# Optimization experiments

Hardware: AMD Instinct MI355X
Metric: run time of the kernel (lower is better)

Reference implementation:

```python
import math
import jax, jax.numpy as jnp
import numpy as np

B, N, M, C, H = 64, 64, 64, 512, 8
HD = C // H
FREQ = 256  # frequency_embedding_size
MAX_PERIOD = 10000.0


def setup_inputs() -> dict:
    key = jax.random.key(0)
    ks = jax.random.split(key, 10)
    s = 1.0 / math.sqrt(C)
    sf = 1.0 / math.sqrt(FREQ)
    return {
        "query": jax.random.normal(ks[0], (B, N, C), jnp.float32),
        "query_pos": jax.random.uniform(ks[1], (1, N, M), jnp.float32),
        # projection weights stored as [in, out]
        "Wq": jax.random.normal(ks[2], (C, C), jnp.float32) * s,
        "bq": jnp.zeros((C,), jnp.float32),
        "Wk": jax.random.normal(ks[3], (C, C), jnp.float32) * s,  # no bias
        "Wv": jax.random.normal(ks[4], (C, C), jnp.float32) * s,
        "bv": jnp.zeros((C,), jnp.float32),
        "Wo": jax.random.normal(ks[5], (C, C), jnp.float32) * s,
        "bo": jnp.zeros((C,), jnp.float32),
        # ScalarEmbedder MLP: Linear(FREQ->C), SiLU, Linear(C->C)
        "W1": jax.random.normal(ks[6], (FREQ, C), jnp.float32) * sf,
        "b1": jnp.zeros((C,), jnp.float32),
        "W2": jax.random.normal(ks[7], (C, C), jnp.float32) * s,
        "b2": jnp.zeros((C,), jnp.float32),
    }


def _freqs():
    half = FREQ // 2
    return jnp.exp(-math.log(MAX_PERIOD) * jnp.arange(half, dtype=jnp.float32) / half)


def reference(query, query_pos, Wq, bq, Wk, Wv, bv, Wo, bo, W1, b1, W2, b2):
    Bq, Nq, Cq = query.shape
    Mk = query_pos.shape[-1]
    # --- ScalarEmbedder on flattened pairwise positions: [N*M] -> [N*M, C]
    t = query_pos.reshape(-1)                       # [Bp*N*M], Bp = 1
    tf = t[:, None] * _freqs()[None, :]             # [N*M, FREQ/2]
    emb = jnp.concatenate([jnp.cos(tf), jnp.sin(tf)], axis=-1)  # [N*M, FREQ]
    pe = jax.nn.silu(emb @ W1 + b1) @ W2 + b2        # [N*M, C]
    pe = pe.reshape(Nq, Mk, H, HD).transpose(2, 0, 1, 3)  # [H, N, M, hd] (tiled over B via broadcast)

    q = (query @ Wq + bq).reshape(Bq, Nq, H, HD)     # bnhd
    k = (query @ Wk).reshape(Bq, Mk, H, HD)          # bmhd (key = query)
    v = (query @ Wv + bv).reshape(Bq, Mk, H, HD)

    scale = HD ** -0.5
    # attn[b,h,n,m] = sum_d q[b,n,h,d] * pe[h,n,m,d] * k[b,m,h,d]
    scores = jnp.einsum("bnhd,hnmd,bmhd->bhnm", q, pe, k) * scale
    attn = jax.nn.softmax(scores, axis=-1)
    x = jnp.einsum("bhnm,bmhd->bnhd", attn, v).reshape(Bq, Nq, Cq)
    return x @ Wo + bo + query  # identity = query
```

## Files before the change

### kernel.cpp

```cpp
#include <hip/hip_runtime.h>
#include <hip/hip_bf16.h>
#include <math.h>

typedef short short8 __attribute__((ext_vector_type(8)));
typedef float floatx4 __attribute__((ext_vector_type(4)));

__device__ __forceinline__ ushort f2bf(float f) {
    __hip_bfloat16 h = __float2bfloat16(f);
    return *reinterpret_cast<ushort*>(&h);
}
__device__ __forceinline__ void bf8_to_f32(uint4 u, float* f) {
    f[0] = __uint_as_float(u.x << 16); f[1] = __uint_as_float(u.x & 0xffff0000u);
    f[2] = __uint_as_float(u.y << 16); f[3] = __uint_as_float(u.y & 0xffff0000u);
    f[4] = __uint_as_float(u.z << 16); f[5] = __uint_as_float(u.z & 0xffff0000u);
    f[6] = __uint_as_float(u.w << 16); f[7] = __uint_as_float(u.w & 0xffff0000u);
}

#define GLDS16(g, l) __builtin_amdgcn_global_load_lds( \
    (const __attribute__((address_space(1))) void*)(g), \
    (__attribute__((address_space(3))) void*)(l), 16, 0, 0)

__global__ __launch_bounds__(256) void prep_kernel(
        const float* __restrict__ W1, const float* __restrict__ W2,
        const float* __restrict__ Wq, const float* __restrict__ Wk,
        const float* __restrict__ Wv, const float* __restrict__ Wo,
        const float* __restrict__ bq, const float* __restrict__ bv,
        const float* __restrict__ query, const float* __restrict__ qpos,
        ushort* __restrict__ W1t, ushort* __restrict__ W2t,
        ushort* __restrict__ Wqkvt, ushort* __restrict__ Wot,
        ushort* __restrict__ queryB, ushort* __restrict__ embB,
        float* __restrict__ biasC) {
    const int z = blockIdx.z;
    const int tx = threadIdx.x, ty = threadIdx.y;
    const int tid = ty * 32 + tx;
    if (z < 6) {
        const float* src; ushort* dst; int R;
        switch (z) {
            case 0:  src = W1; dst = W1t;              R = 256; break;
            case 1:  src = W2; dst = W2t;              R = 512; break;
            case 2:  src = Wq; dst = Wqkvt;            R = 512; break;
            case 3:  src = Wk; dst = Wqkvt + 512*512;  R = 512; break;
            case 4:  src = Wv; dst = Wqkvt + 1024*512; R = 512; break;
            default: src = Wo; dst = Wot;              R = 512; break;
        }
        const int r0 = blockIdx.y * 32, c0 = blockIdx.x * 32;
        if (r0 >= R) return;
        __shared__ float t[32][33];
        for (int i = ty; i < 32; i += 8) t[i][tx] = src[(size_t)(r0 + i) * 512 + c0 + tx];
        __syncthreads();
        for (int i = ty; i < 32; i += 8) dst[(size_t)(c0 + i) * R + r0 + tx] = f2bf(t[tx][i]);
    } else if (z == 6) {
        const int bid = blockIdx.y * 16 + blockIdx.x;
#pragma unroll
        for (int i = 0; i < 8; ++i) {
            size_t idx4 = (size_t)bid * 2048 + i * 256 + tid;
            float4 v = *(const float4*)(query + idx4 * 4);
            ushort4 o; o.x = f2bf(v.x); o.y = f2bf(v.y); o.z = f2bf(v.z); o.w = f2bf(v.w);
            *(ushort4*)(queryB + idx4 * 4) = o;
        }
        if (bid == 0) {
            for (int i = tid; i < 1536; i += 256)
                biasC[i] = (i < 512) ? bq[i] : ((i < 1024) ? 0.0f : bv[i - 1024]);
        }
    } else {
        const int bid = blockIdx.y * 16 + blockIdx.x;
        const int gt = bid * 256 + tid;
        const int e0 = gt * 16;
        const int r = e0 >> 8, j0 = e0 & 255;
        const float t = qpos[r];
        ushort o[16];
#pragma unroll
        for (int u = 0; u < 16; ++u) {
            int j = j0 + u, i = j & 127;
            float freq = __expf(-9.210340371976184f * (float)i * (1.0f / 128.0f));
            float a = t * freq;
            o[u] = f2bf((j < 128) ? __cosf(a) : __sinf(a));
        }
        *(uint4*)(embB + e0)     = *(uint4*)&o[0];
        *(uint4*)(embB + e0 + 8) = *(uint4*)&o[8];
    }
}

__global__ __launch_bounds__(256) void gemm_bf16(
        const ushort* __restrict__ A, const ushort* __restrict__ Bt,
        const float* __restrict__ bias, const float* __restrict__ resid,
        void* __restrict__ Cout, int M, int N, int K, int act, int out_fp32) {
    __shared__ ushort As[64 * 32];
    __shared__ ushort Bs[64 * 32];
    const int tid = threadIdx.x;
    const int l = tid & 63, w = tid >> 6;
    const int wr = w >> 1, wc = w & 1;
    const int row0 = blockIdx.x * 64, col0 = blockIdx.y * 64;
    const int l15 = l & 15, quad = l >> 4;
    const int arow = w * 16 + (l >> 2), koff = (l & 3) * 8;

    const ushort* gA = A  + (size_t)(row0 + arow) * K + koff;
    const ushort* gB = Bt + (size_t)(col0 + arow) * K + koff;
    ushort* lA = &As[w * 512 + l * 8];
    ushort* lB = &Bs[w * 512 + l * 8];

    floatx4 acc[2][2] = {};

    for (int k0 = 0; k0 < K; k0 += 32) {
        __syncthreads();
        GLDS16(gA + k0, lA);
        GLDS16(gB + k0, lB);
        __syncthreads();
        short8 a0 = *(const short8*)&As[(wr * 32 + l15) * 32 + quad * 8];
        short8 a1 = *(const short8*)&As[(wr * 32 + 16 + l15) * 32 + quad * 8];
        short8 b0 = *(const short8*)&Bs[(wc * 32 + l15) * 32 + quad * 8];
        short8 b1 = *(const short8*)&Bs[(wc * 32 + 16 + l15) * 32 + quad * 8];
        acc[0][0] = __builtin_amdgcn_mfma_f32_16x16x32_bf16(a0, b0, acc[0][0], 0, 0, 0);
        acc[0][1] = __builtin_amdgcn_mfma_f32_16x16x32_bf16(a0, b1, acc[0][1], 0, 0, 0);
        acc[1][0] = __builtin_amdgcn_mfma_f32_16x16x32_bf16(a1, b0, acc[1][0], 0, 0, 0);
        acc[1][1] = __builtin_amdgcn_mfma_f32_16x16x32_bf16(a1, b1, acc[1][1], 0, 0, 0);
    }

#pragma unroll
    for (int i = 0; i < 2; ++i)
#pragma unroll
        for (int j = 0; j < 2; ++j) {
            int col = col0 + wc * 32 + j * 16 + l15;
            float bvv = bias ? bias[col] : 0.0f;
#pragma unroll
            for (int r = 0; r < 4; ++r) {
                int row = row0 + wr * 32 + i * 16 + quad * 4 + r;
                float val = acc[i][j][r] + bvv;
                if (act) val = val / (1.0f + __expf(-val));
                if (out_fp32) {
                    float rv = resid ? resid[(size_t)row * N + col] : 0.0f;
                    ((float*)Cout)[(size_t)row * N + col] = val + rv;
                } else {
                    ((ushort*)Cout)[(size_t)row * N + col] = f2bf(val);
                }
            }
        }
}

__global__ __launch_bounds__(256) void attn_bf16(
        const ushort* __restrict__ qkv, const ushort* __restrict__ peB,
        ushort* __restrict__ xB) {
    const int h = blockIdx.x, b = blockIdx.y, nh = blockIdx.z;
    const int tid = threadIdx.x;
    const int w = tid >> 6, l = tid & 63;
    const int lo = l & 7, hi = l >> 3;

    __shared__ float ks[64 * 64];
    __shared__ float vs[64 * 64];
    __shared__ float qs[32 * 64];

#pragma unroll
    for (int p = 0; p < 2; ++p) {
        int cid = p * 256 + tid;
        int row = cid >> 3, ch = cid & 7;
        const ushort* base = qkv + (size_t)(b * 64 + row) * 1536 + h * 64 + ch * 8;
        uint4 ku = *(const uint4*)(base + 512);
        uint4 vu = *(const uint4*)(base + 1024);
        float kf[8], vf[8];
        bf8_to_f32(ku, kf); bf8_to_f32(vu, vf);
#pragma unroll
        for (int j = 0; j < 8; ++j) {
            ks[row * 64 + ch * 8 + j] = kf[j];
            vs[row * 64 + ch * 8 + j] = vf[j];
        }
    }
    {
        int row = tid >> 3, ch = tid & 7;
        uint4 qu = *(const uint4*)(qkv + (size_t)(b * 64 + nh * 32 + row) * 1536 + h * 64 + ch * 8);
        float qf[8]; bf8_to_f32(qu, qf);
#pragma unroll
        for (int j = 0; j < 8; ++j) qs[row * 64 + ch * 8 + j] = qf[j];
    }
    __syncthreads();

    for (int i = 0; i < 8; ++i) {
        int nl = w + 4 * i;
        int n = nh * 32 + nl;
        float qf[8];
        *(float4*)&qf[0] = *(const float4*)&qs[nl * 64 + lo * 8];
        *(float4*)&qf[4] = *(const float4*)&qs[nl * 64 + lo * 8 + 4];

        float sreg[8];
#pragma unroll
        for (int mg = 0; mg < 8; ++mg) {
            int m = mg * 8 + hi;
            uint4 pu = *(const uint4*)(peB + (size_t)(n * 64 + m) * 512 + h * 64 + lo * 8);
            float pf[8]; bf8_to_f32(pu, pf);
            float kf[8];
            *(float4*)&kf[0] = *(const float4*)&ks[m * 64 + lo * 8];
            *(float4*)&kf[4] = *(const float4*)&ks[m * 64 + lo * 8 + 4];
            float p = 0.0f;
#pragma unroll
            for (int j = 0; j < 8; ++j) p = fmaf(qf[j] * kf[j], pf[j], p);
            p += __shfl_xor(p, 1);
            p += __shfl_xor(p, 2);
            p += __shfl_xor(p, 4);
            sreg[mg] = p * 0.125f;
        }

        float mx = sreg[0];
#pragma unroll
        for (int mg = 1; mg < 8; ++mg) mx = fmaxf(mx, sreg[mg]);
        mx = fmaxf(mx, __shfl_xor(mx, 8));
        mx = fmaxf(mx, __shfl_xor(mx, 16));
        mx = fmaxf(mx, __shfl_xor(mx, 32));
        float sum = 0.0f;
#pragma unroll
        for (int mg = 0; mg < 8; ++mg) { sreg[mg] = __expf(sreg[mg] - mx); sum += sreg[mg]; }
        sum += __shfl_xor(sum, 8);
        sum += __shfl_xor(sum, 16);
        sum += __shfl_xor(sum, 32);
        float rs = 1.0f / sum;

        float acc[8] = {};
#pragma unroll
        for (int mg = 0; mg < 8; ++mg) {
            int m = mg * 8 + hi;
            float at = sreg[mg] * rs;
            float vf[8];
            *(float4*)&vf[0] = *(const float4*)&vs[m * 64 + lo * 8];
            *(float4*)&vf[4] = *(const float4*)&vs[m * 64 + lo * 8 + 4];
#pragma unroll
            for (int j = 0; j < 8; ++j) acc[j] = fmaf(at, vf[j], acc[j]);
        }
#pragma unroll
        for (int j = 0; j < 8; ++j) {
            acc[j] += __shfl_xor(acc[j], 8);
            acc[j] += __shfl_xor(acc[j], 16);
            acc[j] += __shfl_xor(acc[j], 32);
        }
        if (l < 8) {
            uint4 o;
            o.x = f2bf(acc[0]) | ((uint)f2bf(acc[1]) << 16);
            o.y = f2bf(acc[2]) | ((uint)f2bf(acc[3]) << 16);
            o.z = f2bf(acc[4]) | ((uint)f2bf(acc[5]) << 16);
            o.w = f2bf(acc[6]) | ((uint)f2bf(acc[7]) << 16);
            *(uint4*)(xB + (size_t)(b * 64 + n) * 512 + h * 64 + l * 8) = o;
        }
    }
}

extern "C" void kernel_launch(void* const* d_in, const int* in_sizes, int n_in,
                              void* d_out, int out_size, void* d_ws, size_t ws_size,
                              hipStream_t stream) {
    const float* query = (const float*)d_in[0];
    const float* qpos  = (const float*)d_in[1];
    const float* Wq    = (const float*)d_in[2];
    const float* bq    = (const float*)d_in[3];
    const float* Wk    = (const float*)d_in[4];
    const float* Wv    = (const float*)d_in[5];
    const float* bv    = (const float*)d_in[6];
    const float* Wo    = (const float*)d_in[7];
    const float* bo    = (const float*)d_in[8];
    const float* W1    = (const float*)d_in[9];
    const float* b1    = (const float*)d_in[10];
    const float* W2    = (const float*)d_in[11];
    const float* b2    = (const float*)d_in[12];
    float* out = (float*)d_out;
    char* ws = (char*)d_ws;

    ushort* W1t    = (ushort*)(ws + 0);
    ushort* W2t    = (ushort*)(ws + 262144);
    ushort* Wqkvt  = (ushort*)(ws + 786432);
    ushort* Wot    = (ushort*)(ws + 2359296);
    float*  biasC  = (float*) (ws + 2883584);
    ushort* embB   = (ushort*)(ws + 3145728);
    ushort* queryB = (ushort*)(ws + 5242880);
    ushort* hiddenB= (ushort*)(ws + 9437184);
    ushort* peB    = (ushort*)(ws + 13631488);
    ushort* qkvB   = (ushort*)(ws + 17825792);
    ushort* xB     = (ushort*)(ws + 30408704);

    prep_kernel<<<dim3(16, 16, 8), dim3(32, 8), 0, stream>>>(
        W1, W2, Wq, Wk, Wv, Wo, bq, bv, query, qpos,
        W1t, W2t, Wqkvt, Wot, queryB, embB, biasC);

    gemm_bf16<<<dim3(64, 8),  256, 0, stream>>>(embB,    W1t,   b1,    nullptr, hiddenB, 4096,  512, 256, 1, 0);
    gemm_bf16<<<dim3(64, 8),  256, 0, stream>>>(hiddenB, W2t,   b2,    nullptr, peB,     4096,  512, 512, 0, 0);
    gemm_bf16<<<dim3(64, 24), 256, 0, stream>>>(queryB,  Wqkvt, biasC, nullptr, qkvB,    4096, 1536, 512, 0, 0);

    attn_bf16<<<dim3(8, 64, 2), 256, 0, stream>>>(qkvB, peB, xB);

    gemm_bf16<<<dim3(64, 8),  256, 0, stream>>>(xB, Wot, bo, query, out, 4096, 512, 512, 0, 1);
}
```

Measured before the change: 163.7 us.

## Replace LDS-staged GEMM and attention with single-wave register-only kernels

The GEMM drops LDS staging and block barriers. Each 64-thread wave now loads its MFMA fragments straight from global memory, with the K dimension and row tiling set as template parameters. The attention kernel also moves to one wave per block, holding K and V in registers instead of shared memory, and splits queries into groups of 8 so there are more blocks. This removes barrier and LDS traffic but gives up reuse across waves in a block, so the same global data is read more times and more registers are needed per thread.

Result: slower. 199.6 us (+21.9%).

```diff
diff --git a/kernel.cpp b/kernel.cpp
--- a/kernel.cpp
+++ b/kernel.cpp
@@ -15,10 +15,6 @@
     f[4] = __uint_as_float(u.z << 16); f[5] = __uint_as_float(u.z & 0xffff0000u);
     f[6] = __uint_as_float(u.w << 16); f[7] = __uint_as_float(u.w & 0xffff0000u);
 }
-
-#define GLDS16(g, l) __builtin_amdgcn_global_load_lds( \
-    (const __attribute__((address_space(1))) void*)(g), \
-    (__attribute__((address_space(3))) void*)(l), 16, 0, 0)
 
 __global__ __launch_bounds__(256) void prep_kernel(
         const float* __restrict__ W1, const float* __restrict__ W2,
@@ -81,50 +77,42 @@
     }
 }
 
-__global__ __launch_bounds__(256) void gemm_bf16(
+template<int K, int TM>
+__global__ __launch_bounds__(64) void gemm_df(
         const ushort* __restrict__ A, const ushort* __restrict__ Bt,
         const float* __restrict__ bias, const float* __restrict__ resid,
-        void* __restrict__ Cout, int M, int N, int K, int act, int out_fp32) {
-    __shared__ ushort As[64 * 32];
-    __shared__ ushort Bs[64 * 32];
-    const int tid = threadIdx.x;
-    const int l = tid & 63, w = tid >> 6;
-    const int wr = w >> 1, wc = w & 1;
-    const int row0 = blockIdx.x * 64, col0 = blockIdx.y * 64;
+        void* __restrict__ Cout, int N, int act, int out_fp32) {
+    const int l = threadIdx.x;
     const int l15 = l & 15, quad = l >> 4;
-    const int arow = w * 16 + (l >> 2), koff = (l & 3) * 8;
-
-    const ushort* gA = A  + (size_t)(row0 + arow) * K + koff;
-    const ushort* gB = Bt + (size_t)(col0 + arow) * K + koff;
-    ushort* lA = &As[w * 512 + l * 8];
-    ushort* lB = &Bs[w * 512 + l * 8];
-
-    floatx4 acc[2][2] = {};
-
+    const int row0 = blockIdx.x * (TM * 16), col0 = blockIdx.y * 64;
+
+    const ushort* pa = A  + (size_t)(row0 + l15) * K + quad * 8;
+    const ushort* pb = Bt + (size_t)(col0 + l15) * K + quad * 8;
+
+    floatx4 acc[TM][4] = {};
+#pragma unroll 2
     for (int k0 = 0; k0 < K; k0 += 32) {
-        __syncthreads();
-        GLDS16(gA + k0, lA);
-        GLDS16(gB + k0, lB);
-        __syncthreads();
-        short8 a0 = *(const short8*)&As[(wr * 32 + l15) * 32 + quad * 8];
-        short8 a1 = *(const short8*)&As[(wr * 32 + 16 + l15) * 32 + quad * 8];
-        short8 b0 = *(const short8*)&Bs[(wc * 32 + l15) * 32 + quad * 8];
-        short8 b1 = *(const short8*)&Bs[(wc * 32 + 16 + l15) * 32 + quad * 8];
-        acc[0][0] = __builtin_amdgcn_mfma_f32_16x16x32_bf16(a0, b0, acc[0][0], 0, 0, 0);
-        acc[0][1] = __builtin_amdgcn_mfma_f32_16x16x32_bf16(a0, b1, acc[0][1], 0, 0, 0);
-        acc[1][0] = __builtin_amdgcn_mfma_f32_16x16x32_bf16(a1, b0, acc[1][0], 0, 0, 0);
-        acc[1][1] = __builtin_amdgcn_mfma_f32_16x16x32_bf16(a1, b1, acc[1][1], 0, 0, 0);
-    }
-
-#pragma unroll
-    for (int i = 0; i < 2; ++i)
-#pragma unroll
-        for (int j = 0; j < 2; ++j) {
-            int col = col0 + wc * 32 + j * 16 + l15;
+        short8 af[TM], bf[4];
+#pragma unroll
+        for (int i = 0; i < TM; ++i) af[i] = *(const short8*)(pa + (size_t)(i * 16) * K + k0);
+#pragma unroll
+        for (int j = 0; j < 4; ++j)  bf[j] = *(const short8*)(pb + (size_t)(j * 16) * K + k0);
+#pragma unroll
+        for (int i = 0; i < TM; ++i)
+#pragma unroll
+            for (int j = 0; j < 4; ++j)
+                acc[i][j] = __builtin_amdgcn_mfma_f32_16x16x32_bf16(af[i], bf[j], acc[i][j], 0, 0, 0);
+    }
+
+#pragma unroll
+    for (int i = 0; i < TM; ++i)
+#pragma unroll
+        for (int j = 0; j < 4; ++j) {
+            int col = col0 + j * 16 + l15;
             float bvv = bias ? bias[col] : 0.0f;
 #pragma unroll
             for (int r = 0; r < 4; ++r) {
-                int row = row0 + wr * 32 + i * 16 + quad * 4 + r;
+                int row = row0 + i * 16 + quad * 4 + r;
                 float val = acc[i][j][r] + bvv;
                 if (act) val = val / (1.0f + __expf(-val));
                 if (out_fp32) {
@@ -137,48 +125,27 @@
         }
 }
 
-__global__ __launch_bounds__(256) void attn_bf16(
+__global__ __launch_bounds__(64) void attn_reg(
         const ushort* __restrict__ qkv, const ushort* __restrict__ peB,
         ushort* __restrict__ xB) {
-    const int h = blockIdx.x, b = blockIdx.y, nh = blockIdx.z;
-    const int tid = threadIdx.x;
-    const int w = tid >> 6, l = tid & 63;
+    const int h = blockIdx.x, b = blockIdx.y, ng = blockIdx.z;
+    const int l = threadIdx.x;
     const int lo = l & 7, hi = l >> 3;
 
-    __shared__ float ks[64 * 64];
-    __shared__ float vs[64 * 64];
-    __shared__ float qs[32 * 64];
-
-#pragma unroll
-    for (int p = 0; p < 2; ++p) {
-        int cid = p * 256 + tid;
-        int row = cid >> 3, ch = cid & 7;
-        const ushort* base = qkv + (size_t)(b * 64 + row) * 1536 + h * 64 + ch * 8;
+    float kr[8][8], vr[8][8];
+#pragma unroll
+    for (int mg = 0; mg < 8; ++mg) {
+        const ushort* base = qkv + (size_t)(b * 64 + mg * 8 + hi) * 1536 + h * 64 + lo * 8;
         uint4 ku = *(const uint4*)(base + 512);
         uint4 vu = *(const uint4*)(base + 1024);
-        float kf[8], vf[8];
-        bf8_to_f32(ku, kf); bf8_to_f32(vu, vf);
-#pragma unroll
-        for (int j = 0; j < 8; ++j) {
-            ks[row * 64 + ch * 8 + j] = kf[j];
-            vs[row * 64 + ch * 8 + j] = vf[j];
-        }
-    }
-    {
-        int row = tid >> 3, ch = tid & 7;
-        uint4 qu = *(const uint4*)(qkv + (size_t)(b * 64 + nh * 32 + row) * 1536 + h * 64 + ch * 8);
+        bf8_to_f32(ku, kr[mg]);
+        bf8_to_f32(vu, vr[mg]);
+    }
+
+    for (int i = 0; i < 8; ++i) {
+        const int n = ng * 8 + i;
+        uint4 qu = *(const uint4*)(qkv + (size_t)(b * 64 + n) * 1536 + h * 64 + lo * 8);
         float qf[8]; bf8_to_f32(qu, qf);
-#pragma unroll
-        for (int j = 0; j < 8; ++j) qs[row * 64 + ch * 8 + j] = qf[j];
-    }
-    __syncthreads();
-
-    for (int i = 0; i < 8; ++i) {
-        int nl = w + 4 * i;
-        int n = nh * 32 + nl;
-        float qf[8];
-        *(float4*)&qf[0] = *(const float4*)&qs[nl * 64 + lo * 8];
-        *(float4*)&qf[4] = *(const float4*)&qs[nl * 64 + lo * 8 + 4];
 
         float sreg[8];
 #pragma unroll
@@ -186,12 +153,9 @@
             int m = mg * 8 + hi;
             uint4 pu = *(const uint4*)(peB + (size_t)(n * 64 + m) * 512 + h * 64 + lo * 8);
             float pf[8]; bf8_to_f32(pu, pf);
-            float kf[8];
-            *(float4*)&kf[0] = *(const float4*)&ks[m * 64 + lo * 8];
-            *(float4*)&kf[4] = *(const float4*)&ks[m * 64 + lo * 8 + 4];
             float p = 0.0f;
 #pragma unroll
-            for (int j = 0; j < 8; ++j) p = fmaf(qf[j] * kf[j], pf[j], p);
+            for (int j = 0; j < 8; ++j) p = fmaf(qf[j] * kr[mg][j], pf[j], p);
             p += __shfl_xor(p, 1);
             p += __shfl_xor(p, 2);
             p += __shfl_xor(p, 4);
@@ -215,13 +179,9 @@
         float acc[8] = {};
 #pragma unroll
         for (int mg = 0; mg < 8; ++mg) {
-            int m = mg * 8 + hi;
             float at = sreg[mg] * rs;
-            float vf[8];
-            *(float4*)&vf[0] = *(const float4*)&vs[m * 64 + lo * 8];
-            *(float4*)&vf[4] = *(const float4*)&vs[m * 64 + lo * 8 + 4];
-#pragma unroll
-            for (int j = 0; j < 8; ++j) acc[j] = fmaf(at, vf[j], acc[j]);
+#pragma unroll
+            for (int j = 0; j < 8; ++j) acc[j] = fmaf(at, vr[mg][j], acc[j]);
         }
 #pragma unroll
         for (int j = 0; j < 8; ++j) {
@@ -275,11 +235,11 @@
         W1, W2, Wq, Wk, Wv, Wo, bq, bv, query, qpos,
         W1t, W2t, Wqkvt, Wot, queryB, embB, biasC);
 
-    gemm_bf16<<<dim3(64, 8),  256, 0, stream>>>(embB,    W1t,   b1,    nullptr, hiddenB, 4096,  512, 256, 1, 0);
-    gemm_bf16<<<dim3(64, 8),  256, 0, stream>>>(hiddenB, W2t,   b2,    nullptr, peB,     4096,  512, 512, 0, 0);
-    gemm_bf16<<<dim3(64, 24), 256, 0, stream>>>(queryB,  Wqkvt, biasC, nullptr, qkvB,    4096, 1536, 512, 0, 0);
-
-    attn_bf16<<<dim3(8, 64, 2), 256, 0, stream>>>(qkvB, peB, xB);
-
-    gemm_bf16<<<dim3(64, 8),  256, 0, stream>>>(xB, Wot, bo, query, out, 4096, 512, 512, 0, 1);
-}
+    gemm_df<256, 2><<<dim3(128, 8),  64, 0, stream>>>(embB,    W1t,   b1,    nullptr, hiddenB, 512,  1, 0);
+    gemm_df<512, 2><<<dim3(128, 8),  64, 0, stream>>>(hiddenB, W2t,   b2,    nullptr, peB,     512,  0, 0);
+    gemm_df<512, 4><<<dim3(64, 24),  64, 0, stream>>>(queryB,  Wqkvt, biasC, nullptr, qkvB,    1536, 0, 0);
+
+    attn_reg<<<dim3(8, 64, 8), 64, 0, stream>>>(qkvB, peB, xB);
+
+    gemm_df<512, 2><<<dim3(128, 8),  64, 0, stream>>>(xB, Wot, bo, query, out, 512, 0, 1);
+}
```
